# Kernel tuning notes

Measured on AMD Instinct MI355X. Metric: run time of the kernel, lower is better.

The kernel has to match this reference:

```python
import jax, jax.numpy as jnp
import numpy as np

POOL = (2, 2)
B, H, W, C = 8, 128, 128, 256
FLAT_OUT = (H * POOL[0]) * (W * POOL[1]) * C  # 16,777,216


def setup_inputs() -> dict:
    key = jax.random.key(0)
    k1, k2 = jax.random.split(key)
    updates = jax.random.normal(k1, (B, H, W, C), dtype=jnp.float32)
    mask = jax.random.randint(k2, (B, H, W, C), 0, FLAT_OUT, dtype=jnp.int32)
    return {"updates": updates, "mask": mask}


def reference(updates, mask):
    ph, pw = POOL
    b, h, w, c = updates.shape
    hout, wout = h * ph, w * pw
    flat_input_size = h * w * c            # NOTE: original uses INPUT size as batch offset
    flat_output_size = hout * wout * c
    # per-batch offset (replicates b * flat_input_size from the TF code)
    batch_range = jnp.arange(b, dtype=jnp.int32).reshape(-1, 1, 1, 1)
    flat_mask = (mask.astype(jnp.int32) + batch_range * flat_input_size).reshape(-1)
    flat_updates = updates.reshape(-1)
    flat_output = jnp.zeros((b * flat_output_size,), dtype=updates.dtype)
    flat_output = flat_output.at[flat_mask].add(flat_updates)
    return flat_output.reshape(b, hout, wout, c)
```

## Files before the change

### kernel.cpp

```cpp
#include <hip/hip_runtime.h>


typedef float floatx4 __attribute__((ext_vector_type(4)));
typedef int   intx4   __attribute__((ext_vector_type(4)));

constexpr int FLAT_IN   = 1 << 22;
constexpr int N_ELEMS   = 8 * FLAT_IN;
constexpr int OUT_WIN   = 7 * FLAT_IN + (1 << 24);
constexpr int OUT_TOTAL = 134217728;

constexpr int CB_SHIFT = 15;
constexpr int NBC      = OUT_WIN >> CB_SHIFT;
constexpr int NBC_PAD  = 1536;
constexpr int WIN_B    = 512;

constexpr int APW      = 1 << CB_SHIFT;
constexpr int NAP      = OUT_TOTAL >> CB_SHIFT;
constexpr int NAP_WIN  = NBC;

constexpr int PBLOCK   = 1024;
constexpr int CHUNK    = 131072;
constexpr int NBLK     = N_ELEMS / CHUNK;
constexpr int ITERS    = CHUNK / (4 * PBLOCK);
constexpr int SEGS     = 8;
constexpr int SEG_ROWS = NBLK / SEGS;

constexpr size_t WS_PAIRS  = 0;
constexpr size_t WS_HISTC  = 268435456;
constexpr size_t WS_SEGC   = WS_HISTC + (size_t)NBLK * NBC_PAD * 4;
constexpr size_t WS_BBC    = WS_SEGC + (size_t)SEGS * NBC_PAD * 4;
constexpr size_t WS_NEEDED = WS_BBC + (size_t)(NBC_PAD + 1) * 4;

__global__ __launch_bounds__(256) void zero_kernel(floatx4* __restrict__ p, int n4) {
  int i = blockIdx.x * 256 + threadIdx.x;
  int stride = gridDim.x * 256;
  floatx4 z = {0.f, 0.f, 0.f, 0.f};
  for (; i < n4; i += stride) __builtin_nontemporal_store(z, p + i);
}

__global__ __launch_bounds__(PBLOCK) void p1_hist(const intx4* __restrict__ mask4,
                                                  int* __restrict__ hist_c) {
  __shared__ int cnt[WIN_B];
  const int blk = blockIdx.x, tid = threadIdx.x;
  if (tid < WIN_B) cnt[tid] = 0;
  __syncthreads();
  const int base4 = blk * (CHUNK / 4);
  #pragma unroll 4
  for (int k = 0; k < ITERS; ++k) {
    intx4 m = mask4[base4 + k * PBLOCK + tid];
    atomicAdd(&cnt[m.x >> CB_SHIFT], 1);
    atomicAdd(&cnt[m.y >> CB_SHIFT], 1);
    atomicAdd(&cnt[m.z >> CB_SHIFT], 1);
    atomicAdd(&cnt[m.w >> CB_SHIFT], 1);
  }
  __syncthreads();
  const int cb0 = ((blk * CHUNK) & ~(FLAT_IN - 1)) >> CB_SHIFT;
  for (int j = tid; j < NBC_PAD; j += PBLOCK) {
    int jj = j - cb0;
    hist_c[blk * NBC_PAD + j] = (jj >= 0 && jj < WIN_B) ? cnt[jj] : 0;
  }
}

__global__ __launch_bounds__(256) void p2_segsum(const int* __restrict__ hist,
                                                 int* __restrict__ segsum) {
  int b = blockIdx.x * 256 + threadIdx.x;
  int seg = blockIdx.y;
  const int* p = hist + (size_t)(seg * SEG_ROWS) * NBC_PAD + b;
  int s = 0;
  #pragma unroll 4
  for (int k = 0; k < SEG_ROWS; ++k) s += p[(size_t)k * NBC_PAD];
  segsum[seg * NBC_PAD + b] = s;
}

__global__ __launch_bounds__(256) void p2_scan_c(const int* __restrict__ segsum,
                                                 int* __restrict__ bbase) {
  __shared__ int tot[NBC_PAD];
  __shared__ int partial[256];
  const int t = threadIdx.x;
  for (int j = t; j < NBC_PAD; j += 256) {
    int s = 0;
    #pragma unroll
    for (int g = 0; g < SEGS; ++g) s += segsum[g * NBC_PAD + j];
    tot[j] = s;
  }
  __syncthreads();
  int local = 0;
  #pragma unroll
  for (int k = 0; k < NBC_PAD / 256; ++k) local += tot[t * (NBC_PAD / 256) + k];
  partial[t] = local;
  __syncthreads();
  for (int off = 1; off < 256; off <<= 1) {
    int tmp = (t >= off) ? partial[t - off] : 0;
    __syncthreads();
    partial[t] += tmp;
    __syncthreads();
  }
  int run = partial[t] - local;
  #pragma unroll
  for (int k = 0; k < NBC_PAD / 256; ++k) {
    int b = t * (NBC_PAD / 256) + k;
    bbase[b] = run;
    run += tot[b];
  }
  if (t == 255) bbase[NBC_PAD] = run;
}

__global__ __launch_bounds__(256) void p2_expand(int* __restrict__ hist,
                                                 const int* __restrict__ segsum) {
  int b = blockIdx.x * 256 + threadIdx.x;
  int seg = blockIdx.y;
  int run = 0;
  for (int g = 0; g < seg; ++g) run += segsum[g * NBC_PAD + b];
  int* p = hist + (size_t)(seg * SEG_ROWS) * NBC_PAD + b;
  for (int k = 0; k < SEG_ROWS; ++k) {
    int v = p[(size_t)k * NBC_PAD];
    p[(size_t)k * NBC_PAD] = run;
    run += v;
  }
}

__global__ __launch_bounds__(PBLOCK) void p3a_place(const intx4* __restrict__ mask4,
                                                    const floatx4* __restrict__ upd4,
                                                    const int* __restrict__ hist_c,
                                                    const int* __restrict__ bbase_c,
                                                    int2* __restrict__ pout) {
  __shared__ int cnt[WIN_B];
  __shared__ int rowbase[WIN_B];
  const int blk = blockIdx.x, tid = threadIdx.x;
  const int boff = (blk * CHUNK) & ~(FLAT_IN - 1);
  const int cb0 = boff >> CB_SHIFT;
  if (tid < WIN_B) {
    cnt[tid] = 0;
    rowbase[tid] = bbase_c[cb0 + tid] + hist_c[blk * NBC_PAD + cb0 + tid];
  }
  __syncthreads();
  const int base4 = blk * (CHUNK / 4);
  #pragma unroll 2
  for (int k = 0; k < ITERS; ++k) {
    int j4 = base4 + k * PBLOCK + tid;
    intx4 m = __builtin_nontemporal_load(mask4 + j4);
    floatx4 u = __builtin_nontemporal_load(upd4 + j4);
    {
      int b = m.x >> CB_SHIFT; int r = atomicAdd(&cnt[b], 1);
      pout[rowbase[b] + r] = make_int2(m.x + boff, __float_as_int(u.x));
    }
    {
      int b = m.y >> CB_SHIFT; int r = atomicAdd(&cnt[b], 1);
      pout[rowbase[b] + r] = make_int2(m.y + boff, __float_as_int(u.y));
    }
    {
      int b = m.z >> CB_SHIFT; int r = atomicAdd(&cnt[b], 1);
      pout[rowbase[b] + r] = make_int2(m.z + boff, __float_as_int(u.z));
    }
    {
      int b = m.w >> CB_SHIFT; int r = atomicAdd(&cnt[b], 1);
      pout[rowbase[b] + r] = make_int2(m.w + boff, __float_as_int(u.w));
    }
  }
}

__global__ __launch_bounds__(1024) void p4c_apply(const int2* __restrict__ pairs,
                                                  const int* __restrict__ bbase,
                                                  float* __restrict__ out) {
  __shared__ float win[APW];
  const int tid = threadIdx.x;
  const int h = blockIdx.x;
  floatx4* w4 = (floatx4*)win;
  floatx4 z = {0.f, 0.f, 0.f, 0.f};
  #pragma unroll
  for (int k = 0; k < APW / 4096; ++k) w4[k * 1024 + tid] = z;
  if (h < NAP_WIN) {
    __syncthreads();
    const int s = bbase[h], e = bbase[h + 1];
    const int s4 = (s + 1) & ~1;
    if ((s & 1) && s < e && tid == 0) {
      int2 p = pairs[s];
      atomicAdd(&win[p.x & (APW - 1)], __int_as_float(p.y));
    }
    const int n2 = (e > s4) ? ((e - s4) >> 1) : 0;
    const intx4* pv = (const intx4*)(pairs + s4);
    for (int i = tid; i < n2; i += 1024) {
      intx4 q = __builtin_nontemporal_load(pv + i);
      atomicAdd(&win[q.x & (APW - 1)], __int_as_float(q.y));
      atomicAdd(&win[q.z & (APW - 1)], __int_as_float(q.w));
    }
    if ((e > s4) && ((e - s4) & 1) && tid == 0) {
      int2 p = pairs[e - 1];
      atomicAdd(&win[p.x & (APW - 1)], __int_as_float(p.y));
    }
    __syncthreads();
  }
  floatx4* o4 = (floatx4*)(out + (size_t)h * APW);
  #pragma unroll
  for (int k = 0; k < APW / 4096; ++k)
    __builtin_nontemporal_store(w4[k * 1024 + tid], o4 + k * 1024 + tid);
}

__global__ __launch_bounds__(256) void scatter_add4_kernel(
    const float4* __restrict__ upd4, const int4* __restrict__ msk4,
    float* __restrict__ out, int n4) {
  int j = blockIdx.x * blockDim.x + threadIdx.x;
  if (j >= n4) return;
  float4 u = upd4[j];
  int4 m = msk4[j];
  int base = (j * 4) & ~(FLAT_IN - 1);
  unsafeAtomicAdd(out + (base + m.x), u.x);
  unsafeAtomicAdd(out + (base + m.y), u.y);
  unsafeAtomicAdd(out + (base + m.z), u.z);
  unsafeAtomicAdd(out + (base + m.w), u.w);
}

extern "C" void kernel_launch(void* const* d_in, const int* in_sizes, int n_in,
                              void* d_out, int out_size, void* d_ws, size_t ws_size,
                              hipStream_t stream) {
  const float* updates = (const float*)d_in[0];
  const int*   mask    = (const int*)d_in[1];
  float*       out     = (float*)d_out;
  const int n = in_sizes[0];

  const bool fast = (n == N_ELEMS) && (out_size == OUT_TOTAL) && (ws_size >= WS_NEEDED);

  if (!fast) {
    int n4z = out_size / 4;
    zero_kernel<<<(n4z + 2047) / 2048, 256, 0, stream>>>((floatx4*)d_out, n4z);
    int n4 = n / 4;
    scatter_add4_kernel<<<(n4 + 255) / 256, 256, 0, stream>>>(
        (const float4*)updates, (const int4*)mask, out, n4);
    return;
  }

  char* ws = (char*)d_ws;
  int2* pairs   = (int2*)(ws + WS_PAIRS);
  int*  hist_c  = (int*)(ws + WS_HISTC);
  int*  segsum  = (int*)(ws + WS_SEGC);
  int*  bbase_c = (int*)(ws + WS_BBC);

  p1_hist<<<NBLK, PBLOCK, 0, stream>>>((const intx4*)mask, hist_c);
  p2_segsum<<<dim3(NBC_PAD / 256, SEGS), 256, 0, stream>>>(hist_c, segsum);
  p2_scan_c<<<1, 256, 0, stream>>>(segsum, bbase_c);
  p2_expand<<<dim3(NBC_PAD / 256, SEGS), 256, 0, stream>>>(hist_c, segsum);
  p3a_place<<<NBLK, PBLOCK, 0, stream>>>((const intx4*)mask, (const floatx4*)updates,
                                         hist_c, bbase_c, pairs);
  p4c_apply<<<NAP, 1024, 0, stream>>>(pairs, bbase_c, out);
}
```

Baseline: 1.133 ms.

## Fuse counting-sort scatter pipeline into one persistent kernel with grid barriers

```diff
diff --git a/kernel.cpp b/kernel.cpp
--- a/kernel.cpp
+++ b/kernel.cpp
@@ -10,26 +10,23 @@
 constexpr int OUT_TOTAL = 134217728;
 
 constexpr int CB_SHIFT = 15;
+constexpr int APW      = 1 << CB_SHIFT;
 constexpr int NBC      = OUT_WIN >> CB_SHIFT;
 constexpr int NBC_PAD  = 1536;
 constexpr int WIN_B    = 512;
-
-constexpr int APW      = 1 << CB_SHIFT;
 constexpr int NAP      = OUT_TOTAL >> CB_SHIFT;
-constexpr int NAP_WIN  = NBC;
-
-constexpr int PBLOCK   = 1024;
-constexpr int CHUNK    = 131072;
-constexpr int NBLK     = N_ELEMS / CHUNK;
-constexpr int ITERS    = CHUNK / (4 * PBLOCK);
-constexpr int SEGS     = 8;
-constexpr int SEG_ROWS = NBLK / SEGS;
+
+constexpr int GRID     = 256;
+constexpr int TPB      = 1024;
+constexpr int CHUNK    = N_ELEMS / GRID;
+constexpr int ITERS    = CHUNK / (4 * TPB);
 
 constexpr size_t WS_PAIRS  = 0;
-constexpr size_t WS_HISTC  = 268435456;
-constexpr size_t WS_SEGC   = WS_HISTC + (size_t)NBLK * NBC_PAD * 4;
-constexpr size_t WS_BBC    = WS_SEGC + (size_t)SEGS * NBC_PAD * 4;
-constexpr size_t WS_NEEDED = WS_BBC + (size_t)(NBC_PAD + 1) * 4;
+constexpr size_t WS_HIST   = 268435456;
+constexpr size_t WS_TOT    = WS_HIST + (size_t)GRID * NBC_PAD * 4;
+constexpr size_t WS_BBASE  = WS_TOT + (size_t)NBC_PAD * 4;
+constexpr size_t WS_BAR    = WS_BBASE + (size_t)(NBC_PAD + 16) * 4;
+constexpr size_t WS_NEEDED = WS_BAR + 64;
 
 __global__ __launch_bounds__(256) void zero_kernel(floatx4* __restrict__ p, int n4) {
   int i = blockIdx.x * 256 + threadIdx.x;
@@ -38,162 +35,158 @@
   for (; i < n4; i += stride) __builtin_nontemporal_store(z, p + i);
 }
 
-__global__ __launch_bounds__(PBLOCK) void p1_hist(const intx4* __restrict__ mask4,
-                                                  int* __restrict__ hist_c) {
-  __shared__ int cnt[WIN_B];
+__device__ __forceinline__ void grid_sync(int* bar, int target) {
+  __syncthreads();
+  if (threadIdx.x == 0) {
+    __threadfence();
+    __hip_atomic_fetch_add(bar, 1, __ATOMIC_ACQ_REL, __HIP_MEMORY_SCOPE_AGENT);
+    while (__hip_atomic_load(bar, __ATOMIC_ACQUIRE, __HIP_MEMORY_SCOPE_AGENT) < target)
+      __builtin_amdgcn_s_sleep(2);
+  }
+  __syncthreads();
+}
+
+__global__ __launch_bounds__(TPB) void mega(const intx4* __restrict__ mask4,
+                                            const floatx4* __restrict__ upd4,
+                                            int* __restrict__ hist,
+                                            int* __restrict__ tot,
+                                            int* __restrict__ bbase,
+                                            int* __restrict__ bar,
+                                            int2* __restrict__ pairs,
+                                            float* __restrict__ out) {
+  __shared__ float win[APW];
+  __shared__ int   cnt[WIN_B];
+  __shared__ int   rowbase[WIN_B];
+  __shared__ int   partial[256];
+
   const int blk = blockIdx.x, tid = threadIdx.x;
-  if (tid < WIN_B) cnt[tid] = 0;
-  __syncthreads();
   const int base4 = blk * (CHUNK / 4);
+  const int boff  = (blk * CHUNK) & ~(FLAT_IN - 1);
+  const int cb0   = boff >> CB_SHIFT;
+
+  for (int j = tid; j < WIN_B; j += TPB) cnt[j] = 0;
+  __syncthreads();
   #pragma unroll 4
   for (int k = 0; k < ITERS; ++k) {
-    intx4 m = mask4[base4 + k * PBLOCK + tid];
+    intx4 m = mask4[base4 + k * TPB + tid];
     atomicAdd(&cnt[m.x >> CB_SHIFT], 1);
     atomicAdd(&cnt[m.y >> CB_SHIFT], 1);
     atomicAdd(&cnt[m.z >> CB_SHIFT], 1);
     atomicAdd(&cnt[m.w >> CB_SHIFT], 1);
   }
   __syncthreads();
-  const int cb0 = ((blk * CHUNK) & ~(FLAT_IN - 1)) >> CB_SHIFT;
-  for (int j = tid; j < NBC_PAD; j += PBLOCK) {
+  for (int j = tid; j < NBC_PAD; j += TPB) {
     int jj = j - cb0;
-    hist_c[blk * NBC_PAD + j] = (jj >= 0 && jj < WIN_B) ? cnt[jj] : 0;
-  }
-}
-
-__global__ __launch_bounds__(256) void p2_segsum(const int* __restrict__ hist,
-                                                 int* __restrict__ segsum) {
-  int b = blockIdx.x * 256 + threadIdx.x;
-  int seg = blockIdx.y;
-  const int* p = hist + (size_t)(seg * SEG_ROWS) * NBC_PAD + b;
-  int s = 0;
-  #pragma unroll 4
-  for (int k = 0; k < SEG_ROWS; ++k) s += p[(size_t)k * NBC_PAD];
-  segsum[seg * NBC_PAD + b] = s;
-}
-
-__global__ __launch_bounds__(256) void p2_scan_c(const int* __restrict__ segsum,
-                                                 int* __restrict__ bbase) {
-  __shared__ int tot[NBC_PAD];
-  __shared__ int partial[256];
-  const int t = threadIdx.x;
-  for (int j = t; j < NBC_PAD; j += 256) {
+    hist[(size_t)blk * NBC_PAD + j] = (jj >= 0 && jj < WIN_B) ? cnt[jj] : 0;
+  }
+  grid_sync(bar, 1 * GRID);
+
+  if (tid < 6) {
+    int j = blk * 6 + tid;
     int s = 0;
-    #pragma unroll
-    for (int g = 0; g < SEGS; ++g) s += segsum[g * NBC_PAD + j];
+    for (int r = 0; r < GRID; ++r) s += hist[(size_t)r * NBC_PAD + j];
     tot[j] = s;
   }
-  __syncthreads();
-  int local = 0;
-  #pragma unroll
-  for (int k = 0; k < NBC_PAD / 256; ++k) local += tot[t * (NBC_PAD / 256) + k];
-  partial[t] = local;
-  __syncthreads();
-  for (int off = 1; off < 256; off <<= 1) {
-    int tmp = (t >= off) ? partial[t - off] : 0;
+  grid_sync(bar, 2 * GRID);
+
+  if (blk == 0) {
+    int local = 0;
+    if (tid < 256) {
+      #pragma unroll
+      for (int k = 0; k < NBC_PAD / 256; ++k) local += tot[tid * (NBC_PAD / 256) + k];
+      partial[tid] = local;
+    }
     __syncthreads();
-    partial[t] += tmp;
-    __syncthreads();
-  }
-  int run = partial[t] - local;
-  #pragma unroll
-  for (int k = 0; k < NBC_PAD / 256; ++k) {
-    int b = t * (NBC_PAD / 256) + k;
-    bbase[b] = run;
-    run += tot[b];
-  }
-  if (t == 255) bbase[NBC_PAD] = run;
-}
-
-__global__ __launch_bounds__(256) void p2_expand(int* __restrict__ hist,
-                                                 const int* __restrict__ segsum) {
-  int b = blockIdx.x * 256 + threadIdx.x;
-  int seg = blockIdx.y;
-  int run = 0;
-  for (int g = 0; g < seg; ++g) run += segsum[g * NBC_PAD + b];
-  int* p = hist + (size_t)(seg * SEG_ROWS) * NBC_PAD + b;
-  for (int k = 0; k < SEG_ROWS; ++k) {
-    int v = p[(size_t)k * NBC_PAD];
-    p[(size_t)k * NBC_PAD] = run;
-    run += v;
-  }
-}
-
-__global__ __launch_bounds__(PBLOCK) void p3a_place(const intx4* __restrict__ mask4,
-                                                    const floatx4* __restrict__ upd4,
-                                                    const int* __restrict__ hist_c,
-                                                    const int* __restrict__ bbase_c,
-                                                    int2* __restrict__ pout) {
-  __shared__ int cnt[WIN_B];
-  __shared__ int rowbase[WIN_B];
-  const int blk = blockIdx.x, tid = threadIdx.x;
-  const int boff = (blk * CHUNK) & ~(FLAT_IN - 1);
-  const int cb0 = boff >> CB_SHIFT;
-  if (tid < WIN_B) {
-    cnt[tid] = 0;
-    rowbase[tid] = bbase_c[cb0 + tid] + hist_c[blk * NBC_PAD + cb0 + tid];
-  }
-  __syncthreads();
-  const int base4 = blk * (CHUNK / 4);
+    for (int off = 1; off < 256; off <<= 1) {
+      int tmp = (tid < 256 && tid >= off) ? partial[tid - off] : 0;
+      __syncthreads();
+      if (tid < 256) partial[tid] += tmp;
+      __syncthreads();
+    }
+    if (tid < 256) {
+      int run = partial[tid] - local;
+      #pragma unroll
+      for (int k = 0; k < NBC_PAD / 256; ++k) {
+        int b = tid * (NBC_PAD / 256) + k;
+        bbase[b] = run;
+        run += tot[b];
+      }
+      if (tid == 255) bbase[NBC_PAD] = run;
+    }
+  }
+  grid_sync(bar, 3 * GRID);
+
+  for (int j = tid; j < WIN_B; j += TPB) {
+    int g = cb0 + j;
+    int run = bbase[g];
+    for (int r = 0; r < blk; ++r) run += hist[(size_t)r * NBC_PAD + g];
+    rowbase[j] = run;
+    cnt[j] = 0;
+  }
+  __syncthreads();
+
   #pragma unroll 2
   for (int k = 0; k < ITERS; ++k) {
-    int j4 = base4 + k * PBLOCK + tid;
+    int j4 = base4 + k * TPB + tid;
     intx4 m = __builtin_nontemporal_load(mask4 + j4);
     floatx4 u = __builtin_nontemporal_load(upd4 + j4);
     {
       int b = m.x >> CB_SHIFT; int r = atomicAdd(&cnt[b], 1);
-      pout[rowbase[b] + r] = make_int2(m.x + boff, __float_as_int(u.x));
+      pairs[rowbase[b] + r] = make_int2(m.x + boff, __float_as_int(u.x));
     }
     {
       int b = m.y >> CB_SHIFT; int r = atomicAdd(&cnt[b], 1);
-      pout[rowbase[b] + r] = make_int2(m.y + boff, __float_as_int(u.y));
+      pairs[rowbase[b] + r] = make_int2(m.y + boff, __float_as_int(u.y));
     }
     {
       int b = m.z >> CB_SHIFT; int r = atomicAdd(&cnt[b], 1);
-      pout[rowbase[b] + r] = make_int2(m.z + boff, __float_as_int(u.z));
+      pairs[rowbase[b] + r] = make_int2(m.z + boff, __float_as_int(u.z));
     }
     {
       int b = m.w >> CB_SHIFT; int r = atomicAdd(&cnt[b], 1);
-      pout[rowbase[b] + r] = make_int2(m.w + boff, __float_as_int(u.w));
-    }
-  }
-}
-
-__global__ __launch_bounds__(1024) void p4c_apply(const int2* __restrict__ pairs,
-                                                  const int* __restrict__ bbase,
-                                                  float* __restrict__ out) {
-  __shared__ float win[APW];
-  const int tid = threadIdx.x;
-  const int h = blockIdx.x;
+      pairs[rowbase[b] + r] = make_int2(m.w + boff, __float_as_int(u.w));
+    }
+  }
+  grid_sync(bar, 4 * GRID);
+
   floatx4* w4 = (floatx4*)win;
   floatx4 z = {0.f, 0.f, 0.f, 0.f};
-  #pragma unroll
-  for (int k = 0; k < APW / 4096; ++k) w4[k * 1024 + tid] = z;
-  if (h < NAP_WIN) {
-    __syncthreads();
-    const int s = bbase[h], e = bbase[h + 1];
-    const int s4 = (s + 1) & ~1;
-    if ((s & 1) && s < e && tid == 0) {
-      int2 p = pairs[s];
-      atomicAdd(&win[p.x & (APW - 1)], __int_as_float(p.y));
-    }
-    const int n2 = (e > s4) ? ((e - s4) >> 1) : 0;
-    const intx4* pv = (const intx4*)(pairs + s4);
-    for (int i = tid; i < n2; i += 1024) {
-      intx4 q = __builtin_nontemporal_load(pv + i);
-      atomicAdd(&win[q.x & (APW - 1)], __int_as_float(q.y));
-      atomicAdd(&win[q.z & (APW - 1)], __int_as_float(q.w));
-    }
-    if ((e > s4) && ((e - s4) & 1) && tid == 0) {
-      int2 p = pairs[e - 1];
-      atomicAdd(&win[p.x & (APW - 1)], __int_as_float(p.y));
-    }
-    __syncthreads();
-  }
-  floatx4* o4 = (floatx4*)(out + (size_t)h * APW);
-  #pragma unroll
-  for (int k = 0; k < APW / 4096; ++k)
-    __builtin_nontemporal_store(w4[k * 1024 + tid], o4 + k * 1024 + tid);
+  #pragma unroll 1
+  for (int i = 0; i < NAP / GRID; ++i) {
+    const int h = i * GRID + blk;
+    floatx4* o4 = (floatx4*)(out + (size_t)h * APW);
+    if (h >= NBC) {
+      #pragma unroll
+      for (int k = 0; k < APW / 4 / TPB; ++k)
+        __builtin_nontemporal_store(z, o4 + k * TPB + tid);
+    } else {
+      __syncthreads();
+      #pragma unroll
+      for (int k = 0; k < APW / 4 / TPB; ++k) w4[k * TPB + tid] = z;
+      __syncthreads();
+      const int s = bbase[h], e = bbase[h + 1];
+      const int s4 = (s + 1) & ~1;
+      if ((s & 1) && s < e && tid == 0) {
+        int2 p = pairs[s];
+        atomicAdd(&win[p.x & (APW - 1)], __int_as_float(p.y));
+      }
+      const int n2 = (e > s4) ? ((e - s4) >> 1) : 0;
+      const intx4* pv = (const intx4*)(pairs + s4);
+      for (int i2 = tid; i2 < n2; i2 += TPB) {
+        intx4 q = __builtin_nontemporal_load(pv + i2);
+        atomicAdd(&win[q.x & (APW - 1)], __int_as_float(q.y));
+        atomicAdd(&win[q.z & (APW - 1)], __int_as_float(q.w));
+      }
+      if ((e > s4) && ((e - s4) & 1) && tid == 0) {
+        int2 p = pairs[e - 1];
+        atomicAdd(&win[p.x & (APW - 1)], __int_as_float(p.y));
+      }
+      __syncthreads();
+      #pragma unroll
+      for (int k = 0; k < APW / 4 / TPB; ++k)
+        __builtin_nontemporal_store(w4[k * TPB + tid], o4 + k * TPB + tid);
+    }
+  }
 }
 
 __global__ __launch_bounds__(256) void scatter_add4_kernel(
@@ -230,16 +223,13 @@
   }
 
   char* ws = (char*)d_ws;
-  int2* pairs   = (int2*)(ws + WS_PAIRS);
-  int*  hist_c  = (int*)(ws + WS_HISTC);
-  int*  segsum  = (int*)(ws + WS_SEGC);
-  int*  bbase_c = (int*)(ws + WS_BBC);
-
-  p1_hist<<<NBLK, PBLOCK, 0, stream>>>((const intx4*)mask, hist_c);
-  p2_segsum<<<dim3(NBC_PAD / 256, SEGS), 256, 0, stream>>>(hist_c, segsum);
-  p2_scan_c<<<1, 256, 0, stream>>>(segsum, bbase_c);
-  p2_expand<<<dim3(NBC_PAD / 256, SEGS), 256, 0, stream>>>(hist_c, segsum);
-  p3a_place<<<NBLK, PBLOCK, 0, stream>>>((const intx4*)mask, (const floatx4*)updates,
-                                         hist_c, bbase_c, pairs);
-  p4c_apply<<<NAP, 1024, 0, stream>>>(pairs, bbase_c, out);
-}
+  int2* pairs = (int2*)(ws + WS_PAIRS);
+  int*  hist  = (int*)(ws + WS_HIST);
+  int*  tot   = (int*)(ws + WS_TOT);
+  int*  bbase = (int*)(ws + WS_BBASE);
+  int*  bar   = (int*)(ws + WS_BAR);
+
+  zero_kernel<<<1, 256, 0, stream>>>((floatx4*)bar, 1);
+  mega<<<GRID, TPB, 0, stream>>>((const intx4*)mask, (const floatx4*)updates,
+                                 hist, tot, bbase, bar, pairs, out);
+}
```

New measurement: 1.399 ms. 23.4% more time.
